# Kernel optimization log

Hardware: AMD Instinct MI355X
Metric: run time of the kernel (lower is better)

Reference implementation:

```python
import jax, jax.numpy as jnp
import numpy as np

N_HEADS = 16

def setup_inputs() -> dict:
    key = jax.random.key(0)
    k1, k2, k3 = jax.random.split(key, 3)
    B, S, D = 4, 2048, 1024
    x = jax.random.normal(k1, (B, S, D), dtype=jnp.float32)
    w_in = jax.random.normal(k2, (D, 3 * D), dtype=jnp.float32) * (1.0 / np.sqrt(D))
    b_in = jnp.zeros((3 * D,), dtype=jnp.float32)
    w_out = jax.random.normal(k3, (D, D), dtype=jnp.float32) * (1.0 / np.sqrt(D))
    b_out = jnp.zeros((D,), dtype=jnp.float32)
    return {"x": x, "w_in": w_in, "b_in": b_in, "w_out": w_out, "b_out": b_out}

def reference(x, w_in, b_in, w_out, b_out):
    B, S, D = x.shape
    H = N_HEADS
    dh = D // H
    qkv = x @ w_in + b_in                      # [B,S,3D]
    q, k, v = jnp.split(qkv, 3, axis=-1)
    # [B,S,D] -> [B,H,S,dh]
    q = q.reshape(B, S, H, dh).transpose(0, 2, 1, 3)
    k = k.reshape(B, S, H, dh).transpose(0, 2, 1, 3)
    v = v.reshape(B, S, H, dh).transpose(0, 2, 1, 3)
    scores = jnp.einsum("bhqd,bhkd->bhqk", q, k) / jnp.sqrt(jnp.float32(dh))
    causal = jnp.tril(jnp.ones((S, S), dtype=bool))  # True = keep
    scores = jnp.where(causal, scores, -jnp.inf)
    attn = jax.nn.softmax(scores, axis=-1)
    out = jnp.einsum("bhqk,bhkd->bhqd", attn, v)
    out = out.transpose(0, 2, 1, 3).reshape(B, S, D)
    out = out @ w_out + b_out
    return (out, (k, v))
```

## Files before the change

kernel.cpp:

```cpp
#include <hip/hip_runtime.h>
#include <hip/hip_bf16.h>
#include <math.h>

typedef __bf16 bf16_t;
typedef __bf16 bf16x2 __attribute__((ext_vector_type(2)));
typedef __bf16 bf16x4 __attribute__((ext_vector_type(4)));
typedef __bf16 bf16x8 __attribute__((ext_vector_type(8)));
typedef float floatx4 __attribute__((ext_vector_type(4)));
typedef unsigned short ushort4v __attribute__((ext_vector_type(4)));

#define AS1 __attribute__((address_space(1)))
#define AS3 __attribute__((address_space(3)))

#define BB 4
#define SS 2048
#define DD 1024
#define HH 16
#define DH 64
#define MM (BB * SS)

__device__ __forceinline__ void gld_lds16(const bf16_t* g, bf16_t* l) {
    __builtin_amdgcn_global_load_lds((const AS1 void*)g, (AS3 void*)l, 16, 0, 0);
}

__global__ void detect_dtype(const unsigned short* __restrict__ x, int* __restrict__ flag) {
    if (threadIdx.x == 0) {
        int hits = 0;
        for (int i = 0; i < 128; ++i) {
            int e = (x[i] >> 7) & 0xFF;
            if (e >= 144) ++hits;
        }
        *flag = (hits >= 4) ? 1 : 0;
    }
}

__global__ __launch_bounds__(256)
void convert_x(const void* __restrict__ in, bf16_t* __restrict__ out,
               const int* __restrict__ flag, int n) {
    const int i4 = (blockIdx.x * 256 + threadIdx.x) * 4;
    if (i4 >= n) return;
    if (*flag) {
        floatx4 v = ((const floatx4*)in)[i4 >> 2];
        out[i4 + 0] = (bf16_t)v[0];
        out[i4 + 1] = (bf16_t)v[1];
        out[i4 + 2] = (bf16_t)v[2];
        out[i4 + 3] = (bf16_t)v[3];
    } else {
        ((ushort4v*)out)[i4 >> 2] = ((const ushort4v*)in)[i4 >> 2];
    }
}

__global__ void convert1d(const void* __restrict__ in, bf16_t* __restrict__ out,
                          const int* __restrict__ flag, int n) {
    const int i = blockIdx.x * 256 + threadIdx.x;
    if (i >= n) return;
    out[i] = (*flag) ? (bf16_t)((const float*)in)[i] : ((const bf16_t*)in)[i];
}

__global__ void transpose_cvt(const void* __restrict__ in, bf16_t* __restrict__ out,
                              const int* __restrict__ flag, int R, int C) {
    __shared__ bf16_t tile[32][33];
    const int tx = threadIdx.x & 31;
    const int ty = threadIdx.x >> 5;
    const int r0 = blockIdx.y * 32;
    const int c0 = blockIdx.x * 32;
    if (*flag) {
        const float* fin = (const float*)in;
#pragma unroll
        for (int i = 0; i < 32; i += 8)
            tile[ty + i][tx] = (bf16_t)fin[(size_t)(r0 + ty + i) * C + (c0 + tx)];
    } else {
        const bf16_t* bin = (const bf16_t*)in;
#pragma unroll
        for (int i = 0; i < 32; i += 8)
            tile[ty + i][tx] = bin[(size_t)(r0 + ty + i) * C + (c0 + tx)];
    }
    __syncthreads();
#pragma unroll
    for (int i = 0; i < 32; i += 8)
        out[(size_t)(c0 + ty + i) * R + (r0 + tx)] = tile[tx][ty + i];
}

#define MFMA8(I, AF)                                                           \
    _Pragma("unroll")                                                          \
    for (int n = 0; n < 4; ++n) {                                              \
        acc[I][n] = __builtin_amdgcn_mfma_f32_16x16x32_bf16(                   \
            AF[0], bfr[n][0], acc[I][n], 0, 0, 0);                             \
        acc[I][n] = __builtin_amdgcn_mfma_f32_16x16x32_bf16(                   \
            AF[1], bfr[n][1], acc[I][n], 0, 0, 0);                             \
    }

template <int MODE>
__global__ __launch_bounds__(512, 2)
void gemm256(const bf16_t* __restrict__ A, const bf16_t* __restrict__ Bt,
             const bf16_t* __restrict__ bias,
             bf16_t* __restrict__ qout, float* __restrict__ kf,
             bf16_t* __restrict__ kb, bf16_t* __restrict__ vtp,
             float* __restrict__ vf, float* __restrict__ outf,
             int nbx, int N) {
    constexpr int KK = 1024;
    constexpr int NT = KK / 64;
    __shared__ bf16_t Ah[4][64 * 64];
    __shared__ bf16_t Bh[4][128 * 64];
    const int tid = threadIdx.x;
    const int w = tid >> 6;
    const int l = tid & 63;
    const int quad = l >> 4;
    const int l16 = l & 15;
    const int wm = w & 1;
    const int wn = w >> 1;

    const int cpx = gridDim.x >> 3;
    const int wg = (blockIdx.x & 7) * cpx + (blockIdx.x >> 3);
    const int m0 = (wg / nbx) * 128;
    const int n0 = (wg % nbx) * 256;

    const int srow = tid >> 3;
    const int sg = (tid & 7) ^ (srow & 7);
    const bf16_t* ag = A + (size_t)(m0 + srow) * KK + sg * 8;
    const bf16_t* bg = Bt + (size_t)(n0 + srow) * KK + sg * 8;
    const int dst0 = w * 512;

    auto stA = [&](int u, int half) {
        gld_lds16(ag + (size_t)half * 64 * KK + u * 64,
                  &Ah[(2 * u + half) & 3][dst0]);
    };
    auto stB = [&](int u, int half) {
        const bf16_t* g = bg + (size_t)half * 128 * KK + u * 64;
        bf16_t* s = &Bh[(2 * u + half) & 3][dst0];
        gld_lds16(g, s);
        gld_lds16(g + (size_t)64 * KK, s + 4096);
    };

    const int axor = l16 & 7;
    auto rdA = [&](int slot, int mt, int kh) -> bf16x8 {
        return *(const bf16x8*)&Ah[slot][(mt * 16 + l16) * 64 +
                                         ((((kh << 2) | quad) ^ axor) << 3)];
    };
    auto rdB = [&](int slot, int nt, int kh) -> bf16x8 {
        return *(const bf16x8*)&Bh[slot][((wn & 1) * 64 + nt * 16 + l16) * 64 +
                                         ((((kh << 2) | quad) ^ axor) << 3)];
    };

    floatx4 acc[4][4];
#pragma unroll
    for (int i = 0; i < 4; ++i)
#pragma unroll
        for (int j = 0; j < 4; ++j) {
            floatx4 z = {0.f, 0.f, 0.f, 0.f};
            acc[i][j] = z;
        }

    bf16x8 bfr[4][2], a0[2], a1[2], a2[2], a3[2];

    stB(0, 0); stB(0, 1); stA(0, 0); stA(0, 1); stB(1, 0); stB(1, 1);
    asm volatile("s_waitcnt vmcnt(4)" ::: "memory");
    __builtin_amdgcn_s_barrier();

    for (int u = 0; u < NT; ++u) {
        const int sa = (2 * u + wm) & 3;
        const int sb = (2 * u + (wn >> 1)) & 3;
        if (u + 1 < NT) { stA(u + 1, 0); stA(u + 1, 1); }
        __builtin_amdgcn_s_barrier();
#pragma unroll
        for (int n = 0; n < 4; ++n) {
            bfr[n][0] = rdB(sb, n, 0);
            bfr[n][1] = rdB(sb, n, 1);
        }
        a0[0] = rdA(sa, 0, 0); a0[1] = rdA(sa, 0, 1);
        MFMA8(0, a0);
        __builtin_amdgcn_s_barrier();
        a1[0] = rdA(sa, 1, 0); a1[1] = rdA(sa, 1, 1);
        MFMA8(1, a1);
        if (u + 2 < NT) stB(u + 2, 0);
        __builtin_amdgcn_s_barrier();
        a2[0] = rdA(sa, 2, 0); a2[1] = rdA(sa, 2, 1);
        a3[0] = rdA(sa, 3, 0); a3[1] = rdA(sa, 3, 1);
        MFMA8(2, a2);
        if (u + 2 < NT) stB(u + 2, 1);
        if (u + 1 < NT) {
            if (u + 2 < NT) asm volatile("s_waitcnt vmcnt(4)" ::: "memory");
            else            asm volatile("s_waitcnt vmcnt(0)" ::: "memory");
        }
        __builtin_amdgcn_s_barrier();
        MFMA8(3, a3);
    }

    const int nb = n0 + wn * 64;
    const int mrow0 = m0 + wm * 64;
    float bv[4];
#pragma unroll
    for (int nt = 0; nt < 4; ++nt) bv[nt] = (float)bias[nb + nt * 16 + l16];

    if (MODE == 0) {
        const int sec = nb >> 10;
        const int c = nb & 1023;
        const int hh = c >> 6;
        const int b = mrow0 >> 11;
        const int sb0 = mrow0 & 2047;
        if (sec == 2) {
#pragma unroll
            for (int mt = 0; mt < 4; ++mt)
#pragma unroll
                for (int nt = 0; nt < 4; ++nt) {
                    const int dcol = nt * 16 + l16;
                    const int sbase = sb0 + mt * 16 + quad * 4;
                    bf16x4 pk;
#pragma unroll
                    for (int r = 0; r < 4; ++r) {
                        const float val = acc[mt][nt][r] + bv[nt];
                        pk[r] = (bf16_t)val;
                        vf[((size_t)(b * HH + hh) * SS + sbase + r) * DH + dcol] = val;
                    }
                    *(bf16x4*)&vtp[((size_t)(b * HH + hh) * DH + dcol) * SS + sbase] = pk;
                }
        } else if (sec == 0) {
#pragma unroll
            for (int mt = 0; mt < 4; ++mt)
#pragma unroll
                for (int nt = 0; nt < 4; ++nt) {
                    const int dcol = nt * 16 + l16;
#pragma unroll
                    for (int r = 0; r < 4; ++r) {
                        const int s = sb0 + mt * 16 + quad * 4 + r;
                        qout[((size_t)(b * HH + hh) * SS + s) * DH + dcol] =
                            (bf16_t)(acc[mt][nt][r] + bv[nt]);
                    }
                }
        } else {
#pragma unroll
            for (int mt = 0; mt < 4; ++mt)
#pragma unroll
                for (int nt = 0; nt < 4; ++nt) {
                    const int dcol = nt * 16 + l16;
#pragma unroll
                    for (int r = 0; r < 4; ++r) {
                        const int s = sb0 + mt * 16 + quad * 4 + r;
                        const size_t di = ((size_t)(b * HH + hh) * SS + s) * DH + dcol;
                        const float val = acc[mt][nt][r] + bv[nt];
                        kf[di] = val;
                        kb[di] = (bf16_t)val;
                    }
                }
        }
    } else {
#pragma unroll
        for (int mt = 0; mt < 4; ++mt)
#pragma unroll
            for (int nt = 0; nt < 4; ++nt)
#pragma unroll
                for (int r = 0; r < 4; ++r) {
                    const int m = mrow0 + mt * 16 + quad * 4 + r;
                    outf[(size_t)m * N + nb + nt * 16 + l16] = acc[mt][nt][r] + bv[nt];
                }
    }
}
#undef MFMA8

#define PST 72

__device__ __forceinline__ void stage_kv(const bf16_t* __restrict__ g, int rstride_e,
                                         bf16_t* l, int tid, int wave) {
#pragma unroll
    for (int half = 0; half < 2; ++half) {
        const int row = half * 32 + (tid >> 3);
        const int srcslot = (tid & 7) ^ (row & 7);
        gld_lds16(g + (size_t)row * rstride_e + srcslot * 8,
                  l + half * 2048 + wave * 512);
    }
}

__device__ __forceinline__ bf16x8 ldsfrag(const bf16_t* base, int row, int s) {
    return *(const bf16x8*)&base[row * 64 + ((s ^ (row & 7)) << 3)];
}

__global__ __launch_bounds__(256)
void flash_v5(const bf16_t* __restrict__ q, const bf16_t* __restrict__ kbf,
              const bf16_t* __restrict__ vt, bf16_t* __restrict__ ao) {
    __shared__ bf16_t Ks[2][64 * 64];
    __shared__ bf16_t Vs[64 * 64];
    __shared__ bf16_t Ps[4][16 * PST];
    const int tid = threadIdx.x;
    const int wave = tid >> 6;
    const int lane = tid & 63;
    const int quad = lane >> 4;
    const int l16 = lane & 15;

    const int linear = blockIdx.x;
    const int xcd = linear & 7;
    const int sl = linear >> 3;
    const int hi = sl & 7;
    const int qt = 31 - (sl >> 3);
    const int bh = xcd * 8 + hi;
    const int r0 = qt * 64 + wave * 16;
    const int b = bh >> 4;
    const int h = bh & 15;

    const bf16_t* qp = q + (size_t)bh * SS * DH;
    const bf16_t* kp = kbf + (size_t)bh * SS * DH;
    const bf16_t* vp = vt + (size_t)bh * DH * SS;
    bf16_t* ps = Ps[wave];

    bf16x8 aq0, aq1;
    {
        const bf16_t* qr = qp + (size_t)(r0 + l16) * DH + quad * 8;
        aq0 = *(const bf16x8*)qr;
        aq1 = *(const bf16x8*)(qr + 32);
    }

    floatx4 o[4];
#pragma unroll
    for (int nt = 0; nt < 4; ++nt) {
        floatx4 z = {0.f, 0.f, 0.f, 0.f};
        o[nt] = z;
    }
    float lrow[4] = {0.f, 0.f, 0.f, 0.f};

    const float c2 = 0.18033688011112042f;
    const float FB = 16.0f;
    const int nIter = qt + 1;

    stage_kv(kp, DH, Ks[0], tid, wave);
    asm volatile("s_waitcnt vmcnt(0)" ::: "memory");
    __builtin_amdgcn_s_barrier();

    int cur = 0;
    for (int it = 0; it < nIter; ++it) {
        const int j0 = it * 64;
        stage_kv(vp + j0, SS, Vs, tid, wave);
        if (it + 1 < nIter)
            stage_kv(kp + (size_t)(j0 + 64) * DH, DH, Ks[cur ^ 1], tid, wave);

        const bf16_t* Kc = Ks[cur];
        floatx4 sc[4];
#pragma unroll
        for (int cp = 0; cp < 4; ++cp) {
            const int krow = (cp >> 1) * 32 + 2 * l16 + (cp & 1);
            const bf16x8 kf0 = ldsfrag(Kc, krow, quad);
            const bf16x8 kf1 = ldsfrag(Kc, krow, 4 + quad);
            floatx4 z = {0.f, 0.f, 0.f, 0.f};
            z = __builtin_amdgcn_mfma_f32_16x16x32_bf16(aq0, kf0, z, 0, 0, 0);
            z = __builtin_amdgcn_mfma_f32_16x16x32_bf16(aq1, kf1, z, 0, 0, 0);
            sc[cp] = z;
        }

        if (it == nIter - 1) {
#pragma unroll
            for (int r = 0; r < 4; ++r) {
                const int qi = r0 + quad * 4 + r;
                float p[4];
#pragma unroll
                for (int cp = 0; cp < 4; ++cp) {
                    const int key = j0 + (cp >> 1) * 32 + 2 * l16 + (cp & 1);
                    const float e = __builtin_amdgcn_exp2f(fmaf(sc[cp][r], c2, -FB));
                    p[cp] = (key <= qi) ? e : 0.f;
                }
                lrow[r] += (p[0] + p[1]) + (p[2] + p[3]);
                const int qrow = quad * 4 + r;
                bf16x2 w0, w1;
                w0[0] = (bf16_t)p[0]; w0[1] = (bf16_t)p[1];
                w1[0] = (bf16_t)p[2]; w1[1] = (bf16_t)p[3];
                *(bf16x2*)&ps[qrow * PST + 2 * l16] = w0;
                *(bf16x2*)&ps[qrow * PST + 32 + 2 * l16] = w1;
            }
        } else {
#pragma unroll
            for (int r = 0; r < 4; ++r) {
                float p[4];
#pragma unroll
                for (int cp = 0; cp < 4; ++cp)
                    p[cp] = __builtin_amdgcn_exp2f(fmaf(sc[cp][r], c2, -FB));
                lrow[r] += (p[0] + p[1]) + (p[2] + p[3]);
                const int qrow = quad * 4 + r;
                bf16x2 w0, w1;
                w0[0] = (bf16_t)p[0]; w0[1] = (bf16_t)p[1];
                w1[0] = (bf16_t)p[2]; w1[1] = (bf16_t)p[3];
                *(bf16x2*)&ps[qrow * PST + 2 * l16] = w0;
                *(bf16x2*)&ps[qrow * PST + 32 + 2 * l16] = w1;
            }
        }
        asm volatile("s_waitcnt lgkmcnt(0)" ::: "memory");
        bf16x8 ap0 = *(const bf16x8*)&ps[l16 * PST + quad * 8];
        bf16x8 ap1 = *(const bf16x8*)&ps[l16 * PST + 32 + quad * 8];

        asm volatile("s_waitcnt vmcnt(0) lgkmcnt(0)" ::: "memory");
        __builtin_amdgcn_s_barrier();

#pragma unroll
        for (int nt = 0; nt < 4; ++nt) {
            const int vrow = nt * 16 + l16;
            const bf16x8 vf0 = ldsfrag(Vs, vrow, quad);
            const bf16x8 vf1 = ldsfrag(Vs, vrow, 4 + quad);
            o[nt] = __builtin_amdgcn_mfma_f32_16x16x32_bf16(ap0, vf0, o[nt], 0, 0, 0);
            o[nt] = __builtin_amdgcn_mfma_f32_16x16x32_bf16(ap1, vf1, o[nt], 0, 0, 0);
        }

        asm volatile("s_waitcnt lgkmcnt(0)" ::: "memory");
        __builtin_amdgcn_s_barrier();
        cur ^= 1;
    }

#pragma unroll
    for (int r = 0; r < 4; ++r) {
#pragma unroll
        for (int off = 1; off < 16; off <<= 1)
            lrow[r] += __shfl_xor(lrow[r], off);
    }
#pragma unroll
    for (int r = 0; r < 4; ++r) {
        const float inv = 1.0f / lrow[r];
        const int s = r0 + quad * 4 + r;
        bf16_t* dst = ao + ((size_t)(b * SS + s) * DD) + h * DH;
#pragma unroll
        for (int nt = 0; nt < 4; ++nt)
            dst[nt * 16 + l16] = (bf16_t)(o[nt][r] * inv);
    }
}
#undef PST

extern "C" void kernel_launch(void* const* d_in, const int* in_sizes, int n_in,
                              void* d_out, int out_size, void* d_ws, size_t ws_size,
                              hipStream_t stream) {
    const void* x_raw = nullptr;
    const void* w_in_raw = nullptr;
    const void* b_in_raw = nullptr;
    const void* w_out_raw = nullptr;
    const void* b_out_raw = nullptr;
    for (int i = 0; i < n_in; ++i) {
        switch (in_sizes[i]) {
            case 8388608: x_raw = d_in[i]; break;
            case 3145728: w_in_raw = d_in[i]; break;
            case 3072:    b_in_raw = d_in[i]; break;
            case 1048576: w_out_raw = d_in[i]; break;
            case 1024:    b_out_raw = d_in[i]; break;
            default: break;
        }
    }

    float* outf  = (float*)d_out;
    float* koutf = outf + (size_t)MM * DD;
    float* voutf = koutf + (size_t)MM * DD;

    bf16_t* q_ws = (bf16_t*)d_out;
    bf16_t* k_bf = q_ws + (size_t)MM * DD;

    char* ws = (char*)d_ws;
    int*    flag    = (int*)ws;
    bf16_t* xc      = (bf16_t*)(ws + 256);
    bf16_t* ao_ws   = xc;
    bf16_t* w_in_t  = (bf16_t*)(ws + 16777472);
    bf16_t* w_out_t = (bf16_t*)(ws + 23068928);
    bf16_t* b_in_c  = (bf16_t*)(ws + 25166080);
    bf16_t* b_out_c = (bf16_t*)(ws + 25172224);
    bf16_t* v_t     = (bf16_t*)(ws + 25174272);

    detect_dtype<<<1, 64, 0, stream>>>((const unsigned short*)x_raw, flag);

    convert_x<<<(MM * DD / 4 + 255) / 256, 256, 0, stream>>>(x_raw, xc, flag, MM * DD);
    transpose_cvt<<<dim3(3 * DD / 32, DD / 32), 256, 0, stream>>>(w_in_raw, w_in_t, flag, DD, 3 * DD);
    transpose_cvt<<<dim3(DD / 32, DD / 32), 256, 0, stream>>>(w_out_raw, w_out_t, flag, DD, DD);
    convert1d<<<(3 * DD + 255) / 256, 256, 0, stream>>>(b_in_raw, b_in_c, flag, 3 * DD);
    convert1d<<<(DD + 255) / 256, 256, 0, stream>>>(b_out_raw, b_out_c, flag, DD);

    gemm256<0><<<dim3(768), 512, 0, stream>>>(
        xc, w_in_t, b_in_c, q_ws, koutf, k_bf, v_t, voutf, nullptr, 12, 3 * DD);

    flash_v5<<<dim3((SS / 64) * BB * HH), 256, 0, stream>>>(q_ws, k_bf, v_t, ao_ws);

    gemm256<1><<<dim3(256), 512, 0, stream>>>(
        ao_ws, w_out_t, b_out_c, nullptr, nullptr, nullptr, nullptr, nullptr,
        outf, 4, DD);
}
```

Baseline: 294.5 us.

## Fuse preprocessing kernels into one launch and raise wave priority around MFMA blocks

Merges dtype detection, x conversion, both weight transposes and bias conversions into one prep kernel. Each block recomputes the dtype flag with a wavefront reduction, so the single-thread detect kernel and five separate launches go away. Also wraps the MFMA sequences in the GEMM and flash-attention loops with s_setprio(1)/s_setprio(0) to favour matrix issue over other waves. The costs are redundant flag loads per block and possible scheduling side effects from the priority changes.

```diff
diff --git a/kernel.cpp b/kernel.cpp
--- a/kernel.cpp
+++ b/kernel.cpp
@@ -23,72 +23,88 @@
     __builtin_amdgcn_global_load_lds((const AS1 void*)g, (AS3 void*)l, 16, 0, 0);
 }
 
-__global__ void detect_dtype(const unsigned short* __restrict__ x, int* __restrict__ flag) {
-    if (threadIdx.x == 0) {
-        int hits = 0;
-        for (int i = 0; i < 128; ++i) {
-            int e = (x[i] >> 7) & 0xFF;
-            if (e >= 144) ++hits;
-        }
-        *flag = (hits >= 4) ? 1 : 0;
-    }
-}
-
 __global__ __launch_bounds__(256)
-void convert_x(const void* __restrict__ in, bf16_t* __restrict__ out,
-               const int* __restrict__ flag, int n) {
-    const int i4 = (blockIdx.x * 256 + threadIdx.x) * 4;
-    if (i4 >= n) return;
-    if (*flag) {
-        floatx4 v = ((const floatx4*)in)[i4 >> 2];
-        out[i4 + 0] = (bf16_t)v[0];
-        out[i4 + 1] = (bf16_t)v[1];
-        out[i4 + 2] = (bf16_t)v[2];
-        out[i4 + 3] = (bf16_t)v[3];
+void prep(const void* __restrict__ x_raw, bf16_t* __restrict__ xc,
+          const void* __restrict__ w_in_raw, bf16_t* __restrict__ w_in_t,
+          const void* __restrict__ w_out_raw, bf16_t* __restrict__ w_out_t,
+          const void* __restrict__ b_in_raw, bf16_t* __restrict__ b_in_c,
+          const void* __restrict__ b_out_raw, bf16_t* __restrict__ b_out_c) {
+    __shared__ bf16_t tile[32][33];
+    __shared__ int sflag;
+    const int tid = threadIdx.x;
+
+    if (tid < 64) {
+        const unsigned short* xs = (const unsigned short*)x_raw;
+        int e0 = (xs[tid * 2] >> 7) & 0xFF;
+        int e1 = (xs[tid * 2 + 1] >> 7) & 0xFF;
+        int h = (e0 >= 144 ? 1 : 0) + (e1 >= 144 ? 1 : 0);
+#pragma unroll
+        for (int off = 1; off < 64; off <<= 1) h += __shfl_xor(h, off);
+        if (tid == 0) sflag = (h >= 4) ? 1 : 0;
+    }
+    __syncthreads();
+    const int flag = sflag;
+
+    const int bid = blockIdx.x;
+    if (bid < 8192) {
+        const int i4 = (bid * 256 + tid) * 4;
+        if (flag) {
+            floatx4 v = ((const floatx4*)x_raw)[i4 >> 2];
+            xc[i4 + 0] = (bf16_t)v[0];
+            xc[i4 + 1] = (bf16_t)v[1];
+            xc[i4 + 2] = (bf16_t)v[2];
+            xc[i4 + 3] = (bf16_t)v[3];
+        } else {
+            ((ushort4v*)xc)[i4 >> 2] = ((const ushort4v*)x_raw)[i4 >> 2];
+        }
+    } else if (bid < 12288) {
+        const void* in;
+        bf16_t* out;
+        int R, C, idx;
+        if (bid < 11264) { in = w_in_raw; out = w_in_t; R = DD; C = 3 * DD; idx = bid - 8192; }
+        else             { in = w_out_raw; out = w_out_t; R = DD; C = DD;   idx = bid - 11264; }
+        const int nbx = C / 32;
+        const int c0 = (idx % nbx) * 32;
+        const int r0 = (idx / nbx) * 32;
+        const int tx = tid & 31;
+        const int ty = tid >> 5;
+        if (flag) {
+            const float* fin = (const float*)in;
+#pragma unroll
+            for (int i = 0; i < 32; i += 8)
+                tile[ty + i][tx] = (bf16_t)fin[(size_t)(r0 + ty + i) * C + (c0 + tx)];
+        } else {
+            const bf16_t* bin = (const bf16_t*)in;
+#pragma unroll
+            for (int i = 0; i < 32; i += 8)
+                tile[ty + i][tx] = bin[(size_t)(r0 + ty + i) * C + (c0 + tx)];
+        }
+        __syncthreads();
+#pragma unroll
+        for (int i = 0; i < 32; i += 8)
+            out[(size_t)(c0 + ty + i) * R + (r0 + tx)] = tile[tx][ty + i];
     } else {
-        ((ushort4v*)out)[i4 >> 2] = ((const ushort4v*)in)[i4 >> 2];
-    }
-}
-
-__global__ void convert1d(const void* __restrict__ in, bf16_t* __restrict__ out,
-                          const int* __restrict__ flag, int n) {
-    const int i = blockIdx.x * 256 + threadIdx.x;
-    if (i >= n) return;
-    out[i] = (*flag) ? (bf16_t)((const float*)in)[i] : ((const bf16_t*)in)[i];
-}
-
-__global__ void transpose_cvt(const void* __restrict__ in, bf16_t* __restrict__ out,
-                              const int* __restrict__ flag, int R, int C) {
-    __shared__ bf16_t tile[32][33];
-    const int tx = threadIdx.x & 31;
-    const int ty = threadIdx.x >> 5;
-    const int r0 = blockIdx.y * 32;
-    const int c0 = blockIdx.x * 32;
-    if (*flag) {
-        const float* fin = (const float*)in;
-#pragma unroll
-        for (int i = 0; i < 32; i += 8)
-            tile[ty + i][tx] = (bf16_t)fin[(size_t)(r0 + ty + i) * C + (c0 + tx)];
-    } else {
-        const bf16_t* bin = (const bf16_t*)in;
-#pragma unroll
-        for (int i = 0; i < 32; i += 8)
-            tile[ty + i][tx] = bin[(size_t)(r0 + ty + i) * C + (c0 + tx)];
-    }
-    __syncthreads();
-#pragma unroll
-    for (int i = 0; i < 32; i += 8)
-        out[(size_t)(c0 + ty + i) * R + (r0 + tx)] = tile[tx][ty + i];
+        const void* in;
+        bf16_t* out;
+        int i;
+        if (bid < 12300) { in = b_in_raw; out = b_in_c; i = (bid - 12288) * 256 + tid; }
+        else             { in = b_out_raw; out = b_out_c; i = (bid - 12300) * 256 + tid; }
+        out[i] = flag ? (bf16_t)((const float*)in)[i] : ((const bf16_t*)in)[i];
+    }
 }
 
 #define MFMA8(I, AF)                                                           \
-    _Pragma("unroll")                                                          \
-    for (int n = 0; n < 4; ++n) {                                              \
-        acc[I][n] = __builtin_amdgcn_mfma_f32_16x16x32_bf16(                   \
-            AF[0], bfr[n][0], acc[I][n], 0, 0, 0);                             \
-        acc[I][n] = __builtin_amdgcn_mfma_f32_16x16x32_bf16(                   \
-            AF[1], bfr[n][1], acc[I][n], 0, 0, 0);                             \
-    }
+    do {                                                                       \
+        __builtin_amdgcn_s_setprio(1);                                         \
+        _Pragma("unroll")                                                      \
+        for (int n = 0; n < 4; ++n) {                                          \
+            acc[I][n] = __builtin_amdgcn_mfma_f32_16x16x32_bf16(               \
+                AF[0], bfr[n][0], acc[I][n], 0, 0, 0);                         \
+            acc[I][n] = __builtin_amdgcn_mfma_f32_16x16x32_bf16(               \
+                AF[1], bfr[n][1], acc[I][n], 0, 0, 0);                         \
+        }                                                                      \
+        __builtin_amdgcn_s_setprio(0);                                         \
+    } while (0)
 
 template <int MODE>
 __global__ __launch_bounds__(512, 2)
@@ -333,6 +349,7 @@
 
         const bf16_t* Kc = Ks[cur];
         floatx4 sc[4];
+        __builtin_amdgcn_s_setprio(1);
 #pragma unroll
         for (int cp = 0; cp < 4; ++cp) {
             const int krow = (cp >> 1) * 32 + 2 * l16 + (cp & 1);
@@ -343,6 +360,7 @@
             z = __builtin_amdgcn_mfma_f32_16x16x32_bf16(aq1, kf1, z, 0, 0, 0);
             sc[cp] = z;
         }
+        __builtin_amdgcn_s_setprio(0);
 
         if (it == nIter - 1) {
 #pragma unroll
@@ -386,6 +404,7 @@
         asm volatile("s_waitcnt vmcnt(0) lgkmcnt(0)" ::: "memory");
         __builtin_amdgcn_s_barrier();
 
+        __builtin_amdgcn_s_setprio(1);
 #pragma unroll
         for (int nt = 0; nt < 4; ++nt) {
             const int vrow = nt * 16 + l16;
@@ -394,6 +413,7 @@
             o[nt] = __builtin_amdgcn_mfma_f32_16x16x32_bf16(ap0, vf0, o[nt], 0, 0, 0);
             o[nt] = __builtin_amdgcn_mfma_f32_16x16x32_bf16(ap1, vf1, o[nt], 0, 0, 0);
         }
+        __builtin_amdgcn_s_setprio(0);
 
         asm volatile("s_waitcnt lgkmcnt(0)" ::: "memory");
         __builtin_amdgcn_s_barrier();
@@ -445,7 +465,6 @@
     bf16_t* k_bf = q_ws + (size_t)MM * DD;
 
     char* ws = (char*)d_ws;
-    int*    flag    = (int*)ws;
     bf16_t* xc      = (bf16_t*)(ws + 256);
     bf16_t* ao_ws   = xc;
     bf16_t* w_in_t  = (bf16_t*)(ws + 16777472);
@@ -454,13 +473,9 @@
     bf16_t* b_out_c = (bf16_t*)(ws + 25172224);
     bf16_t* v_t     = (bf16_t*)(ws + 25174272);
 
-    detect_dtype<<<1, 64, 0, stream>>>((const unsigned short*)x_raw, flag);
-
-    convert_x<<<(MM * DD / 4 + 255) / 256, 256, 0, stream>>>(x_raw, xc, flag, MM * DD);
-    transpose_cvt<<<dim3(3 * DD / 32, DD / 32), 256, 0, stream>>>(w_in_raw, w_in_t, flag, DD, 3 * DD);
-    transpose_cvt<<<dim3(DD / 32, DD / 32), 256, 0, stream>>>(w_out_raw, w_out_t, flag, DD, DD);
-    convert1d<<<(3 * DD + 255) / 256, 256, 0, stream>>>(b_in_raw, b_in_c, flag, 3 * DD);
-    convert1d<<<(DD + 255) / 256, 256, 0, stream>>>(b_out_raw, b_out_c, flag, DD);
+    prep<<<dim3(12304), 256, 0, stream>>>(
+        x_raw, xc, w_in_raw, w_in_t, w_out_raw, w_out_t,
+        b_in_raw, b_in_c, b_out_raw, b_out_c);
 
     gemm256<0><<<dim3(768), 512, 0, stream>>>(
         xc, w_in_t, b_in_c, q_ws, koutf, k_bf, v_t, voutf, nullptr, 12, 3 * DD);
```

Result: no change. 298.6 us (+1.4%).
